# Kernel optimization log

Hardware: AMD Instinct MI355X
Metric: run time of the kernel (lower is better)

The kernel has to match this reference:

```python
import jax, jax.numpy as jnp
import numpy as np

N_NODES = 50000
N_EDGES = 800000
IN_FEAT = 128
HIDDEN = 256
OUT = 64


def setup_inputs() -> dict:
    key = jax.random.key(0)
    ks = jax.random.split(key, 8)
    x = jax.random.normal(ks[0], (N_NODES, IN_FEAT), dtype=jnp.float32)
    edge_index = jax.random.randint(ks[1], (2, N_EDGES), 0, N_NODES, dtype=jnp.int64)
    s1 = 1.0 / np.sqrt(IN_FEAT)
    s2 = 1.0 / np.sqrt(HIDDEN)
    W1_l = jax.random.uniform(ks[2], (HIDDEN, IN_FEAT), jnp.float32, -s1, s1)
    W1_r = jax.random.uniform(ks[3], (HIDDEN, IN_FEAT), jnp.float32, -s1, s1)
    b1 = jax.random.uniform(ks[4], (HIDDEN,), jnp.float32, -s1, s1)
    W2_l = jax.random.uniform(ks[5], (OUT, HIDDEN), jnp.float32, -s2, s2)
    W2_r = jax.random.uniform(ks[6], (OUT, HIDDEN), jnp.float32, -s2, s2)
    b2 = jax.random.uniform(ks[7], (OUT,), jnp.float32, -s2, s2)
    return {"x": x, "edge_index": edge_index, "W1_l": W1_l, "W1_r": W1_r,
            "b1": b1, "W2_l": W2_l, "W2_r": W2_r, "b2": b2}


def _sage_conv(x, src, dst, W_l, W_r, b):
    # mean aggregation of source features onto destination nodes
    msgs = x[src]                                                   # [E, F]
    agg = jax.ops.segment_sum(msgs, dst, num_segments=N_NODES)      # [N, F]
    cnt = jax.ops.segment_sum(jnp.ones((src.shape[0], 1), x.dtype), dst,
                              num_segments=N_NODES)                 # [N, 1]
    agg = agg / jnp.maximum(cnt, 1.0)
    # out = lin_l(agg) + lin_r(x); bias only on lin_l (PyG SAGEConv)
    return agg @ W_l.T + b + x @ W_r.T


def reference(x, edge_index, W1_l, W1_r, b1, W2_l, W2_r, b2):
    src, dst = edge_index[0], edge_index[1]
    h = jax.nn.relu(_sage_conv(x, src, dst, W1_l, W1_r, b1))
    # dropout is identity in eval mode
    return _sage_conv(h, src, dst, W2_l, W2_r, b2)
```

## Files before the change

### kernel.cpp

```cpp
#include <hip/hip_runtime.h>
#include <hip/hip_bf16.h>

#define N_NODES 50000
#define N_EDGES 800000
#define IN_FEAT 128
#define HIDDEN  256
#define OUT_F   64
#define M_PAD   50048
#define CONV_NB 1024
#define GATH_NB 2048
#define NGROUPS 12500
#define BSH     7
#define NBUCK   391
#define NCHUNK  256
#define BCAP    4096

typedef __attribute__((ext_vector_type(8))) short short8;
typedef __attribute__((ext_vector_type(4))) float f32x4;

static __device__ __forceinline__ unsigned short f2bf(float f) {
    unsigned u = __float_as_uint(f);
    unsigned r = (u + 0x7fffu + ((u >> 16) & 1u)) >> 16;
    return (unsigned short)r;
}
static __device__ __forceinline__ float bflo(unsigned u) { return __uint_as_float(u << 16); }
static __device__ __forceinline__ float bfhi(unsigned u) { return __uint_as_float(u & 0xffff0000u); }

__global__ __launch_bounds__(256) void prep_k(const float* __restrict__ x,
                                              unsigned int* __restrict__ A1u,
                                              const float* __restrict__ W1l,
                                              const float* __restrict__ W1r,
                                              unsigned int* __restrict__ Wf1,
                                              const float* __restrict__ W2l,
                                              const float* __restrict__ W2r,
                                              unsigned int* __restrict__ Wf2,
                                              int* __restrict__ gcur) {
    int b = blockIdx.x, t = threadIdx.x;
    if (b < CONV_NB) {
        const int T = CONV_NB * 256;
        const float4* X4 = (const float4*)x;
        for (int i = b * 256 + t; i < N_NODES * 32; i += T) {
            int n = i >> 5, p4 = i & 31;
            float4 v = X4[i];
            unsigned lo = (unsigned)f2bf(v.x) | ((unsigned)f2bf(v.y) << 16);
            unsigned hi = (unsigned)f2bf(v.z) | ((unsigned)f2bf(v.w) << 16);
            unsigned int* dstp = A1u + (size_t)n * 128 + 64 + p4 * 2;
            dstp[0] = lo; dstp[1] = hi;
        }
    } else if (b < CONV_NB + 128) {
        int i = (b - CONV_NB) * 256 + t;
        int s = i * 2;
        int j = s & 7, lane = (s >> 3) & 63, nt = (s >> 9) & 15, ks = s >> 13;
        int n = nt * 16 + (lane & 15);
        int k = ks * 32 + ((lane >> 4) << 3) + j;
        float v0, v1;
        if (k < 128) { v0 = W1l[n * 128 + k];       v1 = W1l[n * 128 + k + 1]; }
        else         { v0 = W1r[n * 128 + k - 128]; v1 = W1r[n * 128 + k - 127]; }
        Wf1[i] = (unsigned)f2bf(v0) | ((unsigned)f2bf(v1) << 16);
    } else if (b < CONV_NB + 128 + 64) {
        int i = (b - CONV_NB - 128) * 256 + t;
        int s = i * 2;
        int j = s & 7, lane = (s >> 3) & 63, nt = (s >> 9) & 7, ks = s >> 12;
        int n = nt * 16 + (lane & 15);
        int k = ks * 32 + ((lane >> 4) << 3) + j;
        float v0, v1;
        if (n < 64) { v0 = W2l[n * 256 + k];        v1 = W2l[n * 256 + k + 1]; }
        else        { v0 = W2r[(n - 64) * 256 + k]; v1 = W2r[(n - 64) * 256 + k + 1]; }
        Wf2[i] = (unsigned)f2bf(v0) | ((unsigned)f2bf(v1) << 16);
    } else {
        for (int i = t; i < NBUCK; i += 256) gcur[i] = 0;
    }
}

__global__ __launch_bounds__(256) void reorder2_k(const int* __restrict__ dst,
                                                  const int* __restrict__ src,
                                                  int* __restrict__ gcur,
                                                  int* __restrict__ ebuf) {
    __shared__ int hist[NBUCK];
    __shared__ int cur[NBUCK];
    int b = blockIdx.x, t = threadIdx.x;
    for (int i = t; i < NBUCK; i += 256) hist[i] = 0;
    __syncthreads();
    for (int e = b * 256 + t; e < N_EDGES; e += NCHUNK * 256)
        atomicAdd(&hist[dst[e] >> BSH], 1);
    __syncthreads();
    for (int i = t; i < NBUCK; i += 256) {
        int h = hist[i];
        cur[i] = (h > 0) ? atomicAdd(&gcur[i], h) : 0;
    }
    __syncthreads();
    for (int e = b * 256 + t; e < N_EDGES; e += NCHUNK * 256) {
        int d = dst[e], sv = src[e];
        int q = d >> BSH;
        int pos = atomicAdd(&cur[q], 1);
        if (pos < BCAP) ebuf[(size_t)q * BCAP + pos] = sv | ((d & 127) << 16);
    }
}

__global__ __launch_bounds__(256) void bucketcsr_k(const int* __restrict__ ebuf,
                                                   const int* __restrict__ gcur,
                                                   int* __restrict__ rowptr,
                                                   int* __restrict__ degv,
                                                   int* __restrict__ eids) {
    __shared__ int ed[BCAP];
    __shared__ int cnt[128];
    __shared__ int s[256];
    __shared__ int cur[128];
    int b = blockIdx.x, t = threadIdx.x;
    int e0 = b * BCAP;
    int m = gcur[b]; if (m > BCAP) m = BCAP;
    int d0 = b << BSH;
    if (t < 128) cnt[t] = 0;
    for (int i = t; i < m; i += 256) ed[i] = ebuf[e0 + i];
    __syncthreads();
    for (int i = t; i < m; i += 256) atomicAdd(&cnt[ed[i] >> 16], 1);
    __syncthreads();
    s[t] = (t < 128) ? cnt[t] : 0;
    __syncthreads();
    for (int off = 1; off < 256; off <<= 1) {
        int add = (t >= off) ? s[t - off] : 0;
        __syncthreads();
        s[t] += add;
        __syncthreads();
    }
    if (t < 128) {
        int excl = s[t] - cnt[t];
        cur[t] = excl;
        int node = d0 + t;
        if (node < N_NODES) { rowptr[node] = e0 + excl; degv[node] = cnt[t]; }
    }
    __syncthreads();
    for (int i = t; i < m; i += 256) {
        int v = ed[i];
        int pos = atomicAdd(&cur[v >> 16], 1);
        eids[e0 + pos] = v & 0xFFFF;
    }
}

__global__ __launch_bounds__(256) void gather1_k(const unsigned int* __restrict__ Au,
                                                 const int* __restrict__ eids,
                                                 const int* __restrict__ rowptr,
                                                 const int* __restrict__ degv,
                                                 unsigned int* __restrict__ Aw) {
    int w = threadIdx.x >> 6, lane = threadIdx.x & 63;
    int eg = lane >> 4, cq = lane & 15;
    for (int g = blockIdx.x; g < NGROUPS; g += GATH_NB) {
        int node = g * 4 + w;
        int b = rowptr[node], e = b + degv[node];
        float a0 = 0.f, a1 = 0.f, a2 = 0.f, a3 = 0.f, a4 = 0.f, a5 = 0.f, a6 = 0.f, a7 = 0.f;
        int i = b + eg;
        for (; i + 12 < e; i += 16) {
            int s0 = eids[i], s1 = eids[i + 4], s2 = eids[i + 8], s3 = eids[i + 12];
            uint4 v0 = ((const uint4*)(Au + (size_t)s0 * 128 + 64))[cq];
            uint4 v1 = ((const uint4*)(Au + (size_t)s1 * 128 + 64))[cq];
            uint4 v2 = ((const uint4*)(Au + (size_t)s2 * 128 + 64))[cq];
            uint4 v3 = ((const uint4*)(Au + (size_t)s3 * 128 + 64))[cq];
            a0 += bflo(v0.x) + bflo(v1.x) + bflo(v2.x) + bflo(v3.x);
            a1 += bfhi(v0.x) + bfhi(v1.x) + bfhi(v2.x) + bfhi(v3.x);
            a2 += bflo(v0.y) + bflo(v1.y) + bflo(v2.y) + bflo(v3.y);
            a3 += bfhi(v0.y) + bfhi(v1.y) + bfhi(v2.y) + bfhi(v3.y);
            a4 += bflo(v0.z) + bflo(v1.z) + bflo(v2.z) + bflo(v3.z);
            a5 += bfhi(v0.z) + bfhi(v1.z) + bfhi(v2.z) + bfhi(v3.z);
            a6 += bflo(v0.w) + bflo(v1.w) + bflo(v2.w) + bflo(v3.w);
            a7 += bfhi(v0.w) + bfhi(v1.w) + bfhi(v2.w) + bfhi(v3.w);
        }
        for (; i < e; i += 4) {
            int s = eids[i];
            uint4 v = ((const uint4*)(Au + (size_t)s * 128 + 64))[cq];
            a0 += bflo(v.x); a1 += bfhi(v.x);
            a2 += bflo(v.y); a3 += bfhi(v.y);
            a4 += bflo(v.z); a5 += bfhi(v.z);
            a6 += bflo(v.w); a7 += bfhi(v.w);
        }
#pragma unroll
        for (int m = 16; m <= 32; m <<= 1) {
            a0 += __shfl_xor(a0, m); a1 += __shfl_xor(a1, m);
            a2 += __shfl_xor(a2, m); a3 += __shfl_xor(a3, m);
            a4 += __shfl_xor(a4, m); a5 += __shfl_xor(a5, m);
            a6 += __shfl_xor(a6, m); a7 += __shfl_xor(a7, m);
        }
        if (eg == 0) {
            int deg = e - b; if (deg < 1) deg = 1;
            float inv = 1.f / (float)deg;
            uint4 r;
            r.x = (unsigned)f2bf(a0 * inv) | ((unsigned)f2bf(a1 * inv) << 16);
            r.y = (unsigned)f2bf(a2 * inv) | ((unsigned)f2bf(a3 * inv) << 16);
            r.z = (unsigned)f2bf(a4 * inv) | ((unsigned)f2bf(a5 * inv) << 16);
            r.w = (unsigned)f2bf(a6 * inv) | ((unsigned)f2bf(a7 * inv) << 16);
            ((uint4*)(Aw + (size_t)node * 128))[cq] = r;
        }
    }
}

__global__ __launch_bounds__(256) void mfma_gemm12_k(
        const unsigned short* __restrict__ A, const unsigned short* __restrict__ Wf1,
        const float* __restrict__ b1, const unsigned short* __restrict__ Wf2,
        const float* __restrict__ b2, unsigned short* __restrict__ y,
        float* __restrict__ out) {
    __shared__ unsigned short hs[64][264];
    int wv = threadIdx.x >> 6, lane = threadIdx.x & 63;
    int row = lane & 15, kg = lane >> 4;

    {
        int rowh = wv >> 1, colh = wv & 1;
        int m0 = blockIdx.x * 64 + rowh * 32;
        const short8* Wf8 = (const short8*)Wf1;
        short8 af[2][8];
#pragma unroll
        for (int mt = 0; mt < 2; mt++) {
            const short8* ar = (const short8*)(A + (size_t)(m0 + mt * 16 + row) * 256 + kg * 8);
#pragma unroll
            for (int ks = 0; ks < 8; ks++) af[mt][ks] = ar[ks * 4];
        }
        f32x4 acc[2][8];
#pragma unroll
        for (int mt = 0; mt < 2; mt++)
#pragma unroll
            for (int nt = 0; nt < 8; nt++) acc[mt][nt] = (f32x4)(0.f);
#pragma unroll
        for (int ks = 0; ks < 8; ks++) {
            short8 bf[8];
#pragma unroll
            for (int nt = 0; nt < 8; nt++)
                bf[nt] = Wf8[(ks * 16 + colh * 8 + nt) * 64 + lane];
#pragma unroll
            for (int nt = 0; nt < 8; nt++) {
#pragma unroll
                for (int mt = 0; mt < 2; mt++)
                    acc[mt][nt] = __builtin_amdgcn_mfma_f32_16x16x32_bf16(af[mt][ks], bf[nt],
                                                                          acc[mt][nt], 0, 0, 0);
            }
        }
#pragma unroll
        for (int mt = 0; mt < 2; mt++) {
            int r0l = rowh * 32 + mt * 16 + kg * 4;
#pragma unroll
            for (int nt = 0; nt < 8; nt++) {
                int c = colh * 128 + nt * 16 + row;
                float bias = b1[c];
#pragma unroll
                for (int i = 0; i < 4; i++) {
                    float v = acc[mt][nt][i] + bias;
                    v = v > 0.f ? v : 0.f;
                    hs[r0l + i][c] = f2bf(v);
                }
            }
        }
    }
    __syncthreads();

    {
        int m0l = wv * 16;
        const short8* Wf8 = (const short8*)Wf2;
        short8 af2[8];
#pragma unroll
        for (int ks = 0; ks < 8; ks++)
            af2[ks] = *(const short8*)(&hs[m0l + row][kg * 8 + ks * 32]);
        f32x4 acc2[8];
#pragma unroll
        for (int nt = 0; nt < 8; nt++) acc2[nt] = (f32x4)(0.f);
#pragma unroll
        for (int ks = 0; ks < 8; ks++) {
            short8 bf[8];
#pragma unroll
            for (int nt = 0; nt < 8; nt++)
                bf[nt] = Wf8[(ks * 8 + nt) * 64 + lane];
#pragma unroll
            for (int nt = 0; nt < 8; nt++)
                acc2[nt] = __builtin_amdgcn_mfma_f32_16x16x32_bf16(af2[ks], bf[nt],
                                                                   acc2[nt], 0, 0, 0);
        }
        int r0 = blockIdx.x * 64 + m0l + kg * 4;
#pragma unroll
        for (int nt = 0; nt < 8; nt++) {
            int c = nt * 16 + row;
#pragma unroll
            for (int i = 0; i < 4; i++) {
                int rr = r0 + i;
                if (nt < 4) {
                    y[(size_t)rr * OUT_F + c] = f2bf(acc2[nt][i]);
                } else if (rr < N_NODES) {
                    out[(size_t)rr * OUT_F + (c - 64)] = acc2[nt][i] + b2[c - 64];
                }
            }
        }
    }
}

__global__ __launch_bounds__(256) void gather2_k(const unsigned int* __restrict__ yu,
                                                 const int* __restrict__ eids,
                                                 const int* __restrict__ rowptr,
                                                 const int* __restrict__ degv,
                                                 float* __restrict__ out) {
    int w = threadIdx.x >> 6, lane = threadIdx.x & 63;
    int eg = lane >> 3, cq = lane & 7;
    for (int g = blockIdx.x; g < NGROUPS; g += GATH_NB) {
        int node = g * 4 + w;
        int b = rowptr[node], e = b + degv[node];
        float a0 = 0.f, a1 = 0.f, a2 = 0.f, a3 = 0.f, a4 = 0.f, a5 = 0.f, a6 = 0.f, a7 = 0.f;
        int i = b + eg;
        for (; i + 8 < e; i += 16) {
            int s0 = eids[i], s1 = eids[i + 8];
            uint4 v0 = ((const uint4*)(yu + (size_t)s0 * 32))[cq];
            uint4 v1 = ((const uint4*)(yu + (size_t)s1 * 32))[cq];
            a0 += bflo(v0.x) + bflo(v1.x); a1 += bfhi(v0.x) + bfhi(v1.x);
            a2 += bflo(v0.y) + bflo(v1.y); a3 += bfhi(v0.y) + bfhi(v1.y);
            a4 += bflo(v0.z) + bflo(v1.z); a5 += bfhi(v0.z) + bfhi(v1.z);
            a6 += bflo(v0.w) + bflo(v1.w); a7 += bfhi(v0.w) + bfhi(v1.w);
        }
        for (; i < e; i += 8) {
            int s = eids[i];
            uint4 v = ((const uint4*)(yu + (size_t)s * 32))[cq];
            a0 += bflo(v.x); a1 += bfhi(v.x);
            a2 += bflo(v.y); a3 += bfhi(v.y);
            a4 += bflo(v.z); a5 += bfhi(v.z);
            a6 += bflo(v.w); a7 += bfhi(v.w);
        }
#pragma unroll
        for (int m = 8; m <= 32; m <<= 1) {
            a0 += __shfl_xor(a0, m); a1 += __shfl_xor(a1, m);
            a2 += __shfl_xor(a2, m); a3 += __shfl_xor(a3, m);
            a4 += __shfl_xor(a4, m); a5 += __shfl_xor(a5, m);
            a6 += __shfl_xor(a6, m); a7 += __shfl_xor(a7, m);
        }
        if (eg == 0) {
            int deg = e - b; if (deg < 1) deg = 1;
            float inv = 1.f / (float)deg;
            float4* p = (float4*)(out + (size_t)node * OUT_F + cq * 8);
            float4 c0 = p[0], c1 = p[1];
            c0.x += a0 * inv; c0.y += a1 * inv; c0.z += a2 * inv; c0.w += a3 * inv;
            c1.x += a4 * inv; c1.y += a5 * inv; c1.z += a6 * inv; c1.w += a7 * inv;
            p[0] = c0; p[1] = c1;
        }
    }
}

extern "C" void kernel_launch(void* const* d_in, const int* in_sizes, int n_in,
                              void* d_out, int out_size, void* d_ws, size_t ws_size,
                              hipStream_t stream) {
    const float* x    = (const float*)d_in[0];
    const int*   eidx = (const int*)d_in[1];
    const float* W1l  = (const float*)d_in[2];
    const float* W1r  = (const float*)d_in[3];
    const float* b1   = (const float*)d_in[4];
    const float* W2l  = (const float*)d_in[5];
    const float* W2r  = (const float*)d_in[6];
    const float* b2   = (const float*)d_in[7];
    float* out = (float*)d_out;

    const int* src = eidx;
    const int* dst = eidx + N_EDGES;

    unsigned short* A1   = (unsigned short*)d_ws;
    unsigned short* ybuf = A1 + (size_t)M_PAD * 256;
    unsigned short* W1f  = ybuf + (size_t)M_PAD * OUT_F;
    unsigned short* W2f  = W1f + 65536;
    int* ebuf   = (int*)(W2f + 32768);
    int* eids   = ebuf + (size_t)NBUCK * BCAP;
    int* rowptr = eids + (size_t)NBUCK * BCAP;
    int* degv   = rowptr + N_NODES;
    int* gcur   = degv + N_NODES;

    prep_k<<<CONV_NB + 128 + 64 + 1, 256, 0, stream>>>(x, (unsigned int*)A1,
                                                       W1l, W1r, (unsigned int*)W1f,
                                                       W2l, W2r, (unsigned int*)W2f, gcur);

    reorder2_k<<<NCHUNK, 256, 0, stream>>>(dst, src, gcur, ebuf);

    bucketcsr_k<<<NBUCK, 256, 0, stream>>>(ebuf, gcur, rowptr, degv, eids);

    gather1_k<<<GATH_NB, 256, 0, stream>>>((const unsigned int*)A1, eids, rowptr, degv,
                                           (unsigned int*)A1);

    mfma_gemm12_k<<<M_PAD / 64, 256, 0, stream>>>(A1, W1f, b1, W2f, b2, ybuf, out);

    gather2_k<<<GATH_NB, 256, 0, stream>>>((const unsigned int*)ybuf, eids, rowptr, degv, out);
}
```

Baseline: 122.7 us.

## Fuse bucket CSR build with first-layer neighbor gather

Merges the bucket-to-CSR kernel and the first gather into one kernel launched with two 512-thread blocks per bucket. Each block rebuilds the bucket's sorted edge list in shared memory and gathers features for its half of the bucket's 128 nodes, reading source ids from LDS rather than global memory. This drops one launch and the global round trip of eids before the first gather. The cost is that the sorting work is done twice per bucket and LDS use per block roughly doubles, which can lower occupancy.

```diff
diff --git a/kernel.cpp b/kernel.cpp
--- a/kernel.cpp
+++ b/kernel.cpp
@@ -97,60 +97,66 @@
     }
 }
 
-__global__ __launch_bounds__(256) void bucketcsr_k(const int* __restrict__ ebuf,
-                                                   const int* __restrict__ gcur,
-                                                   int* __restrict__ rowptr,
-                                                   int* __restrict__ degv,
-                                                   int* __restrict__ eids) {
+__global__ __launch_bounds__(512) void bcsr_gather1_k(
+        const int* __restrict__ ebuf, const int* __restrict__ gcur,
+        const unsigned int* __restrict__ Au,
+        int* __restrict__ rowptr, int* __restrict__ degv, int* __restrict__ eids,
+        unsigned int* __restrict__ Aw) {
     __shared__ int ed[BCAP];
+    __shared__ int led[BCAP];
     __shared__ int cnt[128];
-    __shared__ int s[256];
+    __shared__ int loff[128];
     __shared__ int cur[128];
-    int b = blockIdx.x, t = threadIdx.x;
+    __shared__ int sc[128];
+    int blk = blockIdx.x;
+    int b = blk >> 1, half = blk & 1;
+    int t = threadIdx.x;
     int e0 = b * BCAP;
     int m = gcur[b]; if (m > BCAP) m = BCAP;
     int d0 = b << BSH;
     if (t < 128) cnt[t] = 0;
-    for (int i = t; i < m; i += 256) ed[i] = ebuf[e0 + i];
-    __syncthreads();
-    for (int i = t; i < m; i += 256) atomicAdd(&cnt[ed[i] >> 16], 1);
-    __syncthreads();
-    s[t] = (t < 128) ? cnt[t] : 0;
-    __syncthreads();
-    for (int off = 1; off < 256; off <<= 1) {
-        int add = (t >= off) ? s[t - off] : 0;
+    for (int i = t; i < m; i += 512) ed[i] = ebuf[e0 + i];
+    __syncthreads();
+    for (int i = t; i < m; i += 512) atomicAdd(&cnt[ed[i] >> 16], 1);
+    __syncthreads();
+    if (t < 128) sc[t] = cnt[t];
+    __syncthreads();
+    for (int off = 1; off < 128; off <<= 1) {
+        int v = 0;
+        if (t < 128 && t >= off) v = sc[t - off];
         __syncthreads();
-        s[t] += add;
+        if (t < 128) sc[t] += v;
         __syncthreads();
     }
     if (t < 128) {
-        int excl = s[t] - cnt[t];
+        int excl = sc[t] - cnt[t];
+        loff[t] = excl;
         cur[t] = excl;
         int node = d0 + t;
-        if (node < N_NODES) { rowptr[node] = e0 + excl; degv[node] = cnt[t]; }
-    }
-    __syncthreads();
-    for (int i = t; i < m; i += 256) {
+        if (half == 0 && node < N_NODES) { rowptr[node] = e0 + excl; degv[node] = cnt[t]; }
+    }
+    __syncthreads();
+    for (int i = t; i < m; i += 512) {
         int v = ed[i];
         int pos = atomicAdd(&cur[v >> 16], 1);
-        eids[e0 + pos] = v & 0xFFFF;
-    }
-}
-
-__global__ __launch_bounds__(256) void gather1_k(const unsigned int* __restrict__ Au,
-                                                 const int* __restrict__ eids,
-                                                 const int* __restrict__ rowptr,
-                                                 const int* __restrict__ degv,
-                                                 unsigned int* __restrict__ Aw) {
-    int w = threadIdx.x >> 6, lane = threadIdx.x & 63;
+        led[pos] = v & 0xFFFF;
+    }
+    __syncthreads();
+    if (half == 0)
+        for (int i = t; i < m; i += 512) eids[e0 + i] = led[i];
+
+    int wv = t >> 6, lane = t & 63;
     int eg = lane >> 4, cq = lane & 15;
-    for (int g = blockIdx.x; g < NGROUPS; g += GATH_NB) {
-        int node = g * 4 + w;
-        int b = rowptr[node], e = b + degv[node];
+#pragma unroll 1
+    for (int j = 0; j < 8; j++) {
+        int nl = half * 64 + wv * 8 + j;
+        int node = d0 + nl;
+        if (node >= N_NODES) continue;
+        int bo = loff[nl], e = bo + cnt[nl];
         float a0 = 0.f, a1 = 0.f, a2 = 0.f, a3 = 0.f, a4 = 0.f, a5 = 0.f, a6 = 0.f, a7 = 0.f;
-        int i = b + eg;
+        int i = bo + eg;
         for (; i + 12 < e; i += 16) {
-            int s0 = eids[i], s1 = eids[i + 4], s2 = eids[i + 8], s3 = eids[i + 12];
+            int s0 = led[i], s1 = led[i + 4], s2 = led[i + 8], s3 = led[i + 12];
             uint4 v0 = ((const uint4*)(Au + (size_t)s0 * 128 + 64))[cq];
             uint4 v1 = ((const uint4*)(Au + (size_t)s1 * 128 + 64))[cq];
             uint4 v2 = ((const uint4*)(Au + (size_t)s2 * 128 + 64))[cq];
@@ -165,7 +171,7 @@
             a7 += bfhi(v0.w) + bfhi(v1.w) + bfhi(v2.w) + bfhi(v3.w);
         }
         for (; i < e; i += 4) {
-            int s = eids[i];
+            int s = led[i];
             uint4 v = ((const uint4*)(Au + (size_t)s * 128 + 64))[cq];
             a0 += bflo(v.x); a1 += bfhi(v.x);
             a2 += bflo(v.y); a3 += bfhi(v.y);
@@ -173,14 +179,14 @@
             a6 += bflo(v.w); a7 += bfhi(v.w);
         }
 #pragma unroll
-        for (int m = 16; m <= 32; m <<= 1) {
-            a0 += __shfl_xor(a0, m); a1 += __shfl_xor(a1, m);
-            a2 += __shfl_xor(a2, m); a3 += __shfl_xor(a3, m);
-            a4 += __shfl_xor(a4, m); a5 += __shfl_xor(a5, m);
-            a6 += __shfl_xor(a6, m); a7 += __shfl_xor(a7, m);
+        for (int mm = 16; mm <= 32; mm <<= 1) {
+            a0 += __shfl_xor(a0, mm); a1 += __shfl_xor(a1, mm);
+            a2 += __shfl_xor(a2, mm); a3 += __shfl_xor(a3, mm);
+            a4 += __shfl_xor(a4, mm); a5 += __shfl_xor(a5, mm);
+            a6 += __shfl_xor(a6, mm); a7 += __shfl_xor(a7, mm);
         }
         if (eg == 0) {
-            int deg = e - b; if (deg < 1) deg = 1;
+            int deg = e - bo; if (deg < 1) deg = 1;
             float inv = 1.f / (float)deg;
             uint4 r;
             r.x = (unsigned)f2bf(a0 * inv) | ((unsigned)f2bf(a1 * inv) << 16);
@@ -367,10 +373,8 @@
 
     reorder2_k<<<NCHUNK, 256, 0, stream>>>(dst, src, gcur, ebuf);
 
-    bucketcsr_k<<<NBUCK, 256, 0, stream>>>(ebuf, gcur, rowptr, degv, eids);
-
-    gather1_k<<<GATH_NB, 256, 0, stream>>>((const unsigned int*)A1, eids, rowptr, degv,
-                                           (unsigned int*)A1);
+    bcsr_gather1_k<<<NBUCK * 2, 512, 0, stream>>>(ebuf, gcur, (const unsigned int*)A1,
+                                                  rowptr, degv, eids, (unsigned int*)A1);
 
     mfma_gemm12_k<<<M_PAD / 64, 256, 0, stream>>>(A1, W1f, b1, W2f, b2, ybuf, out);
 
```

New measurement: 119.3 us. -2.8%, faster.
